# Optimization experiments

Hardware: AMD Instinct MI355X
Metric: run time of the kernel (lower is better)

The kernel has to match this reference:

```python
import jax, jax.numpy as jnp
import numpy as np
from jax.scipy.special import logsumexp

NEG = -1e30  # log-zero surrogate (avoids inf arithmetic)
DEN_SCALE = 1.0


def setup_inputs() -> dict:
    key = jax.random.key(0)
    k1, k2_, k3, k4 = jax.random.split(key, 4)
    B, T, C, L = 64, 2000, 256, 128
    nnet_output = jax.random.normal(k1, (B, T, C), dtype=jnp.float32)
    trans = jax.random.normal(k2_, (C, C), dtype=jnp.float32) * 0.1
    labels = jax.random.randint(k3, (B, L), 0, C, dtype=jnp.int32)
    # durations >= 1024 so the length-L numerator chain is always reachable
    durations = (1024 + jax.random.randint(k4, (B,), 0, T - 1024)).astype(jnp.int32)
    return {"nnet_output": nnet_output, "trans": trans, "labels": labels,
            "durations": durations}


def _lfmmi_scores(nnet_output, trans, labels, durations):
    """Log-semiring forward DP: numerator (linear label chain w/ self-loops)
    and denominator (dense bigram FSA over all symbols). Returns per-utt
    num - den_scale * den, as in num_tot_scores - den_scale*den_tot_scores."""
    B, T, C = nnet_output.shape
    L = labels.shape[1]
    x = jnp.moveaxis(nnet_output, 1, 0)            # [T, B, C]

    # ---- numerator: alpha over label positions [B, L] ----
    emit0 = jnp.take_along_axis(x[0], labels, axis=1)      # [B, L]
    alpha0 = jnp.full((B, L), NEG, x.dtype).at[:, 0].set(emit0[:, 0])

    def num_step(alpha, tx):
        t, x_t = tx
        emit = jnp.take_along_axis(x_t, labels, axis=1)     # [B, L]
        shifted = jnp.concatenate(
            [jnp.full((B, 1), NEG, alpha.dtype), alpha[:, :-1]], axis=1)
        new = jnp.logaddexp(alpha, shifted) + emit          # self-loop | advance
        active = (t < durations)[:, None]
        return jnp.where(active, new, alpha), None

    ts = jnp.arange(1, T)
    alpha, _ = jax.lax.scan(num_step, alpha0, (ts, x[1:]))
    num_score = alpha[:, -1]                                # [B]

    # ---- denominator: beta over symbols [B, C], dense bigram transitions ----
    beta0 = x[0]

    def den_step(beta, tx):
        t, x_t = tx
        # [B, C_prev, 1] + [1, C_prev, C_next] -> logsumexp over prev
        new = logsumexp(beta[:, :, None] + trans[None, :, :], axis=1) + x_t
        active = (t < durations)[:, None]
        return jnp.where(active, new, beta), None

    beta, _ = jax.lax.scan(den_step, beta0, (ts, x[1:]))
    den_score = logsumexp(beta, axis=1)                     # [B]

    return num_score - DEN_SCALE * den_score


def reference(nnet_output, trans, labels, durations):
    tot_scores = _lfmmi_scores(nnet_output, trans, labels, durations)  # [B]
    tot_frames = jnp.sum(durations)
    # get_tot_objf_and_num_frames: sum of (finite) per-utt scores, frame counts
    tot_score = jnp.sum(tot_scores)
    return tot_score, tot_frames, tot_frames
```

## Files before the change

### kernel.cpp

```cpp
#include <hip/hip_runtime.h>

#define NEGV -1e30f
constexpr int Bn = 64, Tn = 2000, Cn = 256, Ln = 128;

__device__ __forceinline__ float wave_max(float v) {
#pragma unroll
  for (int s = 32; s; s >>= 1) v = fmaxf(v, __shfl_xor(v, s, 64));
  return v;
}
__device__ __forceinline__ float wave_sum(float v) {
#pragma unroll
  for (int s = 32; s; s >>= 1) v += __shfl_xor(v, s, 64);
  return v;
}
__device__ __forceinline__ unsigned int bf16_rne(float f) {
  return (__float_as_uint(f) + 0x8000u) >> 16;
}

__global__ __launch_bounds__(512, 1) void lfmmi_main(
    const float* __restrict__ nnet, const float* __restrict__ trans,
    const int* __restrict__ labels, const int* __restrict__ durs,
    float* __restrict__ den_out, float* __restrict__ num_out) {
  __shared__ __align__(16) float part[8][Cn];
  __shared__ __align__(16) unsigned short p_bf[Cn];
  __shared__ float m_lds[2];
  const int tid = threadIdx.x;
  const int blk = blockIdx.x;

  if (blk < Bn) {
    const int b = blk;
    const int dur = durs[b];
    const int w = tid >> 6;
    const int lane = tid & 63;

    unsigned int Eu[16][4];
#pragma unroll
    for (int k = 0; k < 16; ++k) {
#pragma unroll
      for (int c = 0; c < 4; ++c) {
        const int i0 = w * 32 + 2 * k;
        const int j = lane * 4 + c;
        const unsigned int lo = bf16_rne(__expf(trans[i0 * Cn + j]));
        const unsigned int hi = bf16_rne(__expf(trans[(i0 + 1) * Cn + j]));
        Eu[k][c] = (lo & 0xffffu) | (hi << 16);
      }
    }

    const float* xb = nnet + (size_t)b * Tn * Cn;
    const bool is_red = (tid < Cn);
    float beta = 0.f, m_carry = 0.f, xn1 = 0.f, xn2 = 0.f;
    if (is_red) {
      beta = xb[tid];
      m_carry = xb[0];
      p_bf[tid] = (unsigned short)bf16_rne(__expf(beta - m_carry));
      if (tid == 0) m_lds[0] = beta;
      xn1 = xb[Cn + tid];
      xn2 = xb[2 * Cn + tid];
    }
    __syncthreads();

    for (int t = 1; t < dur; ++t) {
      const float m_new = is_red ? m_lds[(t - 1) & 1] : 0.f;

      union { uint4 q[4]; unsigned int u[16]; } P;
      const uint4* psrc = (const uint4*)&p_bf[w * 32];
      P.q[0] = psrc[0]; P.q[1] = psrc[1]; P.q[2] = psrc[2]; P.q[3] = psrc[3];

      float acc[4] = {0.f, 0.f, 0.f, 0.f};
#pragma unroll
      for (int k = 0; k < 16; ++k) {
#pragma unroll
        for (int c = 0; c < 4; ++c) {
          asm("v_dot2_f32_bf16 %0, %1, %2, %0"
              : "+v"(acc[c]) : "v"(P.u[k]), "v"(Eu[k][c]));
        }
      }
      *(float4*)&part[w][lane * 4] =
          make_float4(acc[0], acc[1], acc[2], acc[3]);
      __syncthreads();

      if (is_red) {
        float s = part[0][tid];
#pragma unroll
        for (int q = 1; q < 8; ++q) s += part[q][tid];
        beta = m_carry + __logf(s) + xn1;
        xn1 = xn2;
        const int tn = (t + 2 < Tn) ? t + 2 : Tn - 1;
        xn2 = xb[(size_t)tn * Cn + tid];
        m_carry = m_new;
        p_bf[tid] = (unsigned short)bf16_rne(__expf(beta - m_carry));
        if (tid == 0) m_lds[t & 1] = beta;
      }
      __syncthreads();
    }

    if (is_red) part[0][tid] = beta;
    __syncthreads();
    if (tid < 64) {
      const float4 v = ((const float4*)part[0])[tid];
      float mx = fmaxf(fmaxf(v.x, v.y), fmaxf(v.z, v.w));
      mx = wave_max(mx);
      float sm = __expf(v.x - mx) + __expf(v.y - mx) +
                 __expf(v.z - mx) + __expf(v.w - mx);
      sm = wave_sum(sm);
      if (tid == 0) den_out[b] = mx + __logf(sm);
    }
  } else {
    const int b = blk - Bn;
    if (tid >= 64) return;
    const int dur = durs[b];
    const int lane = tid;
    const float* xb = nnet + (size_t)b * Tn * Cn;
    const int lab0 = labels[b * Ln + lane];
    const int lab1 = labels[b * Ln + 64 + lane];
    float a0 = (lane == 0) ? xb[lab0] : NEGV;
    float a1 = NEGV;
    float ea1 = xb[(size_t)1 * Cn + lab0], eb1 = xb[(size_t)1 * Cn + lab1];
    float ea2 = xb[(size_t)2 * Cn + lab0], eb2 = xb[(size_t)2 * Cn + lab1];
    float ea3 = xb[(size_t)3 * Cn + lab0], eb3 = xb[(size_t)3 * Cn + lab1];
    float ea4 = xb[(size_t)4 * Cn + lab0], eb4 = xb[(size_t)4 * Cn + lab1];

    for (int t = 1; t < dur; ++t) {
      const float ec0 = ea1, ec1 = eb1;
      ea1 = ea2; ea2 = ea3; ea3 = ea4;
      eb1 = eb2; eb2 = eb3; eb3 = eb4;
      const int tn = (t + 4 < Tn) ? t + 4 : Tn - 1;
      ea4 = xb[(size_t)tn * Cn + lab0];
      eb4 = xb[(size_t)tn * Cn + lab1];

      const float p0s = __shfl_up(a0, 1, 64);
      const float p1s = __shfl_up(a1, 1, 64);
      const float w63 = __shfl(a0, 63, 64);
      const float prev0 = lane ? p0s : NEGV;
      const float prev1 = lane ? p1s : w63;

      const float mx0 = fmaxf(a0, prev0), d0 = fminf(a0, prev0) - mx0;
      const float mx1 = fmaxf(a1, prev1), d1 = fminf(a1, prev1) - mx1;
      a0 = mx0 + log1pf(__expf(d0)) + ec0;
      a1 = mx1 + log1pf(__expf(d1)) + ec1;
    }
    if (lane == 63) num_out[b] = a1;
  }
}

__global__ void lfmmi_final(const float* __restrict__ den,
                            const float* __restrict__ num,
                            const int* __restrict__ durs,
                            float* __restrict__ out) {
  const int tid = threadIdx.x;
  float v = num[tid] - den[tid];
  float d = (float)durs[tid];
  v = wave_sum(v);
  d = wave_sum(d);
  if (tid == 0) {
    out[0] = v;
    out[1] = d;
    out[2] = d;
  }
}

extern "C" void kernel_launch(void* const* d_in, const int* in_sizes, int n_in,
                              void* d_out, int out_size, void* d_ws, size_t ws_size,
                              hipStream_t stream) {
  const float* nnet = (const float*)d_in[0];
  const float* trans = (const float*)d_in[1];
  const int* labels = (const int*)d_in[2];
  const int* durs = (const int*)d_in[3];
  float* den_ws = (float*)d_ws;
  float* num_ws = den_ws + Bn;
  lfmmi_main<<<dim3(2 * Bn), dim3(512), 0, stream>>>(nnet, trans, labels, durs,
                                                     den_ws, num_ws);
  lfmmi_final<<<dim3(1), dim3(64), 0, stream>>>(den_ws, num_ws, durs,
                                                (float*)d_out);
}
```

Baseline: 1.299 ms.

## Repartition den matvec so each output reduces in-wave, drop one barrier per step

The dense bigram matvec is re-split so each wave owns 32 output columns, and the two half-waves each cover half of the previous-symbol range. The partial sums are combined with a single cross-half shuffle, which removes the LDS partial-sum array and the intermediate barrier. p_bf becomes double-buffered so only one __syncthreads per timestep is needed. Every thread now computes beta redundantly (two lanes per column), and each thread keeps 64 packed registers of transition weights.

```diff
diff --git a/kernel.cpp b/kernel.cpp
--- a/kernel.cpp
+++ b/kernel.cpp
@@ -21,8 +21,8 @@
     const float* __restrict__ nnet, const float* __restrict__ trans,
     const int* __restrict__ labels, const int* __restrict__ durs,
     float* __restrict__ den_out, float* __restrict__ num_out) {
-  __shared__ __align__(16) float part[8][Cn];
-  __shared__ __align__(16) unsigned short p_bf[Cn];
+  __shared__ __align__(16) unsigned short p_bf[2][Cn];
+  __shared__ __align__(16) float fin[Cn];
   __shared__ float m_lds[2];
   const int tid = threadIdx.x;
   const int blk = blockIdx.x;
@@ -32,72 +32,62 @@
     const int dur = durs[b];
     const int w = tid >> 6;
     const int lane = tid & 63;
+    const int c = lane & 31;
+    const int h = lane >> 5;
+    const int j = w * 32 + c;
 
-    unsigned int Eu[16][4];
+    unsigned int Ep[64];
 #pragma unroll
-    for (int k = 0; k < 16; ++k) {
-#pragma unroll
-      for (int c = 0; c < 4; ++c) {
-        const int i0 = w * 32 + 2 * k;
-        const int j = lane * 4 + c;
-        const unsigned int lo = bf16_rne(__expf(trans[i0 * Cn + j]));
-        const unsigned int hi = bf16_rne(__expf(trans[(i0 + 1) * Cn + j]));
-        Eu[k][c] = (lo & 0xffffu) | (hi << 16);
-      }
+    for (int k = 0; k < 64; ++k) {
+      const int i0 = 128 * h + 2 * k;
+      const unsigned int lo = bf16_rne(__expf(trans[i0 * Cn + j]));
+      const unsigned int hi = bf16_rne(__expf(trans[(i0 + 1) * Cn + j]));
+      Ep[k] = (lo & 0xffffu) | (hi << 16);
     }
 
     const float* xb = nnet + (size_t)b * Tn * Cn;
-    const bool is_red = (tid < Cn);
-    float beta = 0.f, m_carry = 0.f, xn1 = 0.f, xn2 = 0.f;
-    if (is_red) {
-      beta = xb[tid];
-      m_carry = xb[0];
-      p_bf[tid] = (unsigned short)bf16_rne(__expf(beta - m_carry));
-      if (tid == 0) m_lds[0] = beta;
-      xn1 = xb[Cn + tid];
-      xn2 = xb[2 * Cn + tid];
-    }
+    float beta = xb[j];
+    const float m0 = xb[0];
+    float m_add = m0;
+    if (h == 0) p_bf[1][j] = (unsigned short)bf16_rne(__expf(beta - m0));
+    if (tid == 0) m_lds[0] = m0;
+    float xn1 = xb[Cn + j];
+    float xn2 = xb[2 * Cn + j];
     __syncthreads();
 
     for (int t = 1; t < dur; ++t) {
-      const float m_new = is_red ? m_lds[(t - 1) & 1] : 0.f;
+      const int cur = t & 1;
+      const float mn = m_lds[(t - 1) & 1];
 
-      union { uint4 q[4]; unsigned int u[16]; } P;
-      const uint4* psrc = (const uint4*)&p_bf[w * 32];
-      P.q[0] = psrc[0]; P.q[1] = psrc[1]; P.q[2] = psrc[2]; P.q[3] = psrc[3];
-
-      float acc[4] = {0.f, 0.f, 0.f, 0.f};
+      const uint4* ps = (const uint4*)&p_bf[cur][128 * h];
+      float a0 = 0.f, a1 = 0.f, a2 = 0.f, a3 = 0.f;
 #pragma unroll
       for (int k = 0; k < 16; ++k) {
-#pragma unroll
-        for (int c = 0; c < 4; ++c) {
-          asm("v_dot2_f32_bf16 %0, %1, %2, %0"
-              : "+v"(acc[c]) : "v"(P.u[k]), "v"(Eu[k][c]));
-        }
+        const uint4 q = ps[k];
+        asm("v_dot2_f32_bf16 %0, %1, %2, %0" : "+v"(a0) : "v"(q.x), "v"(Ep[4 * k + 0]));
+        asm("v_dot2_f32_bf16 %0, %1, %2, %0" : "+v"(a1) : "v"(q.y), "v"(Ep[4 * k + 1]));
+        asm("v_dot2_f32_bf16 %0, %1, %2, %0" : "+v"(a2) : "v"(q.z), "v"(Ep[4 * k + 2]));
+        asm("v_dot2_f32_bf16 %0, %1, %2, %0" : "+v"(a3) : "v"(q.w), "v"(Ep[4 * k + 3]));
       }
-      *(float4*)&part[w][lane * 4] =
-          make_float4(acc[0], acc[1], acc[2], acc[3]);
-      __syncthreads();
+      float s = (a0 + a1) + (a2 + a3);
+      s += __shfl_xor(s, 32, 64);
+      beta = m_add + __logf(s) + xn1;
 
-      if (is_red) {
-        float s = part[0][tid];
-#pragma unroll
-        for (int q = 1; q < 8; ++q) s += part[q][tid];
-        beta = m_carry + __logf(s) + xn1;
-        xn1 = xn2;
-        const int tn = (t + 2 < Tn) ? t + 2 : Tn - 1;
-        xn2 = xb[(size_t)tn * Cn + tid];
-        m_carry = m_new;
-        p_bf[tid] = (unsigned short)bf16_rne(__expf(beta - m_carry));
-        if (tid == 0) m_lds[t & 1] = beta;
-      }
+      xn1 = xn2;
+      const int tn = (t + 2 < Tn) ? t + 2 : Tn - 1;
+      xn2 = xb[(size_t)tn * Cn + j];
+
+      if (h == 0)
+        p_bf[cur ^ 1][j] = (unsigned short)bf16_rne(__expf(beta - mn));
+      if (tid == 0) m_lds[t & 1] = beta;
+      m_add = mn;
       __syncthreads();
     }
 
-    if (is_red) part[0][tid] = beta;
+    if (h == 0) fin[j] = beta;
     __syncthreads();
     if (tid < 64) {
-      const float4 v = ((const float4*)part[0])[tid];
+      const float4 v = ((const float4*)fin)[tid];
       float mx = fmaxf(fmaxf(v.x, v.y), fmaxf(v.z, v.w));
       mx = wave_max(mx);
       float sm = __expf(v.x - mx) + __expf(v.y - mx) +
```

Result: no change. 1.288 ms (-0.8%).
